# Kernel optimization log

Measured on AMD Instinct MI355X. Metric: run time of the kernel, lower is better.

## Reference

```python
import jax, jax.numpy as jnp
import numpy as np


def setup_inputs() -> dict:
    key = jax.random.key(0)
    k1, k2, k3, k4 = jax.random.split(key, 4)
    B, N, C_IN, C_OUT, K = 8, 4096, 64, 64, 16
    H = W = 64  # H * W == N
    x = jax.random.normal(k1, (B, N, C_IN), dtype=jnp.float32)
    edge_index = jax.random.randint(k2, (B, N, K), 0, N, dtype=jnp.int64)
    # 1x1 Conv2d(2*C_IN -> C_OUT) is a [C_OUT, 2*C_IN] matmul + bias
    weight = jax.random.normal(k3, (C_OUT, 2 * C_IN), dtype=jnp.float32) * 0.05
    bias = jax.random.normal(k4, (C_OUT,), dtype=jnp.float32) * 0.01
    return {"x": x, "edge_index": edge_index, "weight": weight, "bias": bias,
            "H": H, "W": W}


def reference(x, edge_index, weight, bias, H, W):
    # x: [B, N, C], edge_index: [B, N, K] with values in [0, N)
    B, N, C = x.shape
    K = edge_index.shape[-1]
    # Gather neighbor features per batch element (batched index_select)
    idx = edge_index.reshape(B, N * K, 1)                      # [B, N*K, 1]
    neighbors = jnp.take_along_axis(x, idx, axis=1)            # [B, N*K, C]
    neighbors = neighbors.reshape(B, N, K, C)                  # [B, N, K, C]
    x_central = x[:, :, None, :]                               # [B, N, 1, C]
    # edge feature: concat([x_i, x_j - x_i]) -> [B, N, K, 2C]
    edge_feat = jnp.concatenate(
        [jnp.broadcast_to(x_central, (B, N, K, C)), neighbors - x_central],
        axis=-1)
    # 1x1 conv + ReLU
    out = jax.nn.relu(jnp.einsum('bnkc,oc->bnko', edge_feat, weight) + bias)
    # max over neighbors k -> [B, N, C_out]
    out = jnp.max(out, axis=2)
    # [B, C_out, N] -> [B, C_out, H, W]
    return jnp.transpose(out, (0, 2, 1)).reshape(B, weight.shape[0], H, W)
```

## Files before the change

kernel.cpp:

```cpp
#include <hip/hip_runtime.h>
#include <stdint.h>

#define B_SZ    8
#define N_PTS   4096
#define C_IN    64
#define C_OUT   64
#define KNN     16
#define ROWS    (B_SZ * N_PTS)

typedef __attribute__((ext_vector_type(8))) short v8s;
typedef __attribute__((ext_vector_type(4))) float v4f;

__device__ inline unsigned short f2bf(float f) {
    unsigned int u = __float_as_uint(f);
    return (unsigned short)((u + 0x7FFFu + ((u >> 16) & 1u)) >> 16);
}

__global__ __launch_bounds__(256) void wprep_kernel(const float* __restrict__ w,
                                                    v8s* __restrict__ wfrag)
{
    __shared__ float wl[2 * C_IN * C_OUT];
    const int t = threadIdx.x;
    {
        const float4* src = (const float4*)w;
        float4*       dst = (float4*)wl;
#pragma unroll
        for (int i = 0; i < 8; ++i)
            dst[i * 256 + t] = src[i * 256 + t];
    }
    __syncthreads();

    const int tid  = blockIdx.x * 256 + t;
    const int lane = tid & 63;
    const int ks   = (tid >> 6) & 1;
    const int ct   = tid >> 7;
    const int col  = ct * 16 + (lane & 15);
    const int kb   = ks * 32 + 8 * (lane >> 4);

    v8s f;
#pragma unroll
    for (int j = 0; j < 8; ++j) {
        const int k = kb + j;
        const float v = (col < 64)
            ? (wl[col * 128 + k] - wl[col * 128 + 64 + k])
            : wl[(col - 64) * 128 + 64 + k];
        f[j] = (short)f2bf(v);
    }
    wfrag[tid] = f;
}

__global__ __launch_bounds__(256, 2) void proj_nbuf(
    const float* __restrict__ x,
    const v8s*  __restrict__ wfrag,
    unsigned short* __restrict__ nbuf)
{
    const int lane  = threadIdx.x & 63;
    const int wv    = threadIdx.x >> 6;
    const int batch = blockIdx.x & 7;
    const int chunk = blockIdx.x >> 3;
    const int r0    = batch * N_PTS + chunk * 64 + wv * 16;

    v8s bfrag[4][2];
#pragma unroll
    for (int ct = 0; ct < 4; ++ct)
#pragma unroll
        for (int ks = 0; ks < 2; ++ks)
            bfrag[ct][ks] = wfrag[((4 + ct) * 2 + ks) * 64 + lane];

    const int arow = r0 + (lane & 15);
    const int koff = 8 * (lane >> 4);
    v8s afrag[2];
#pragma unroll
    for (int ks = 0; ks < 2; ++ks) {
        const float* xp = x + (size_t)arow * C_IN + ks * 32 + koff;
        const float4 q0 = *(const float4*)xp;
        const float4 q1 = *(const float4*)(xp + 4);
        v8s a;
        a[0] = (short)f2bf(q0.x); a[1] = (short)f2bf(q0.y);
        a[2] = (short)f2bf(q0.z); a[3] = (short)f2bf(q0.w);
        a[4] = (short)f2bf(q1.x); a[5] = (short)f2bf(q1.y);
        a[6] = (short)f2bf(q1.z); a[7] = (short)f2bf(q1.w);
        afrag[ks] = a;
    }

    v4f acc[4];
#pragma unroll
    for (int ct = 0; ct < 4; ++ct)
        acc[ct] = (v4f){0.f, 0.f, 0.f, 0.f};

#pragma unroll
    for (int ks = 0; ks < 2; ++ks)
#pragma unroll
        for (int ct = 0; ct < 4; ++ct)
            acc[ct] = __builtin_amdgcn_mfma_f32_16x16x32_bf16(
                afrag[ks], bfrag[ct][ks], acc[ct], 0, 0, 0);

    const int crow0 = r0 + (lane >> 4) * 4;
    const int ccol  = lane & 15;
#pragma unroll
    for (int ct = 0; ct < 4; ++ct)
#pragma unroll
        for (int reg = 0; reg < 4; ++reg)
            nbuf[(size_t)(crow0 + reg) * C_OUT + ct * 16 + ccol] =
                f2bf(acc[ct][reg]);
}

#define PITCH 68

__global__ __launch_bounds__(256) void gather_fused(
    const float* __restrict__ x,
    const v8s*  __restrict__ wfrag,
    const float* __restrict__ bias,
    const int* __restrict__ eidx,
    const unsigned short* __restrict__ nbuf,
    float* __restrict__ out)
{
    __shared__ float sm[32][PITCH];

    const int t    = threadIdx.x;
    const int lane = t & 63;
    const int wv   = t >> 6;
    const int b    = blockIdx.x & 7;
    const int tn   = blockIdx.x >> 3;
    const int n0   = tn * 32;
    const int r0g  = b * N_PTS + n0;

    {
        const float4* xsrc = (const float4*)(x + (size_t)r0g * C_IN);
#pragma unroll
        for (int i = 0; i < 2; ++i) {
            const int idx = i * 256 + t;
            *(float4*)&sm[idx >> 4][(idx & 15) * 4] = xsrc[idx];
        }
    }
    __syncthreads();

    const int rq  = wv & 1;
    const int ch  = wv >> 1;
    const int rl0 = rq * 16;

    v8s bfrag[2][2];
#pragma unroll
    for (int ct = 0; ct < 2; ++ct)
#pragma unroll
        for (int ks = 0; ks < 2; ++ks)
            bfrag[ct][ks] = wfrag[((ch * 2 + ct) * 2 + ks) * 64 + lane];

    const int rl   = rl0 + (lane & 15);
    const int koff = 8 * (lane >> 4);
    v8s afrag[2];
#pragma unroll
    for (int ks = 0; ks < 2; ++ks) {
        const float* xp = &sm[rl][ks * 32 + koff];
        const float4 q0 = *(const float4*)xp;
        const float4 q1 = *(const float4*)(xp + 4);
        v8s a;
        a[0] = (short)f2bf(q0.x); a[1] = (short)f2bf(q0.y);
        a[2] = (short)f2bf(q0.z); a[3] = (short)f2bf(q0.w);
        a[4] = (short)f2bf(q1.x); a[5] = (short)f2bf(q1.y);
        a[6] = (short)f2bf(q1.z); a[7] = (short)f2bf(q1.w);
        afrag[ks] = a;
    }

    v4f acc[2];
#pragma unroll
    for (int ct = 0; ct < 2; ++ct) {
        const float bv = bias[ch * 32 + ct * 16 + (lane & 15)];
        acc[ct] = (v4f){bv, bv, bv, bv};
    }
#pragma unroll
    for (int ks = 0; ks < 2; ++ks)
#pragma unroll
        for (int ct = 0; ct < 2; ++ct)
            acc[ct] = __builtin_amdgcn_mfma_f32_16x16x32_bf16(
                afrag[ks], bfrag[ct][ks], acc[ct], 0, 0, 0);

    __syncthreads();

    const int orow = rl0 + (lane >> 4) * 4;
    const int ccol = lane & 15;
#pragma unroll
    for (int ct = 0; ct < 2; ++ct)
#pragma unroll
        for (int reg = 0; reg < 4; ++reg)
            sm[orow + reg][ch * 32 + ct * 16 + ccol] = acc[ct][reg];

    __syncthreads();

    const unsigned short* nb = nbuf + (size_t)b * N_PTS * C_OUT;
    const int o4  = (lane & 15) * 4;
    const int sub = lane >> 4;

#pragma unroll
    for (int i = 0; i < 2; ++i) {
        const int rbl   = wv * 8 + i * 4;
        const int rbase = r0g + rbl;
        int myidx = eidx[(size_t)rbase * KNN + lane] & (N_PTS - 1);

        const float4 cv = *(const float4*)&sm[rbl + sub][o4];

        float m0 = -1e30f, m1 = -1e30f, m2 = -1e30f, m3 = -1e30f;
#pragma unroll
        for (int k = 0; k < KNN; ++k) {
            const int idx = __shfl(myidx, (lane & 48) | k);
            const uint2 v = *(const uint2*)(nb + (size_t)idx * C_OUT + o4);
            m0 = fmaxf(m0, __uint_as_float(v.x << 16));
            m1 = fmaxf(m1, __uint_as_float(v.x & 0xffff0000u));
            m2 = fmaxf(m2, __uint_as_float(v.y << 16));
            m3 = fmaxf(m3, __uint_as_float(v.y & 0xffff0000u));
        }

        const int nl = rbl + sub;
        sm[nl][o4 + 0] = fmaxf(cv.x + m0, 0.f);
        sm[nl][o4 + 1] = fmaxf(cv.y + m1, 0.f);
        sm[nl][o4 + 2] = fmaxf(cv.z + m2, 0.f);
        sm[nl][o4 + 3] = fmaxf(cv.w + m3, 0.f);
    }

    __syncthreads();

    float* ob = out + (size_t)b * C_OUT * N_PTS + n0;
    const int nn = lane & 31;
    const int oh = lane >> 5;
#pragma unroll
    for (int j = 0; j < 8; ++j) {
        const int o = wv * 16 + j * 2 + oh;
        ob[(size_t)o * N_PTS + nn] = sm[nn][o];
    }
}

extern "C" void kernel_launch(void* const* d_in, const int* in_sizes, int n_in,
                              void* d_out, int out_size, void* d_ws, size_t ws_size,
                              hipStream_t stream)
{
    const float* x    = (const float*)d_in[0];
    const int*   eidx = (const int*)d_in[1];
    const float* w    = (const float*)d_in[2];
    const float* bias = (const float*)d_in[3];
    float*       out  = (float*)d_out;

    unsigned short* nbuf  = (unsigned short*)d_ws;
    v8s*            wfrag = (v8s*)((char*)d_ws + (size_t)ROWS * C_OUT * 2);

    wprep_kernel<<<4, 256, 0, stream>>>(w, wfrag);
    proj_nbuf<<<ROWS / 64, 256, 0, stream>>>(x, wfrag, nbuf);
    gather_fused<<<B_SZ * (N_PTS / 32), 256, 0, stream>>>(x, wfrag, bias, eidx,
                                                          nbuf, out);
}
```

Baseline: 20.76 us.

## Fold weight prep into consumer kernels and drop separate wprep launch

Removes the wprep kernel and has each consumer kernel load weights from global memory and build its bf16 MFMA fragments directly, including the W1-W2 subtraction in gather_fused. proj_nbuf is restructured to 32-row tiles staged through shared memory with two column tiles per wave, and launch bounds are raised to 4 blocks per SM. Edge indices are prefetched at the start of gather_fused so their latency overlaps the x tile load, and one barrier is removed. The aim is to cut one launch and its serialization, at the cost of redundant per-block weight loads and conversions.

```diff
diff --git a/kernel.cpp b/kernel.cpp
--- a/kernel.cpp
+++ b/kernel.cpp
@@ -16,100 +16,90 @@
     return (unsigned short)((u + 0x7FFFu + ((u >> 16) & 1u)) >> 16);
 }
 
-__global__ __launch_bounds__(256) void wprep_kernel(const float* __restrict__ w,
-                                                    v8s* __restrict__ wfrag)
-{
-    __shared__ float wl[2 * C_IN * C_OUT];
-    const int t = threadIdx.x;
-    {
-        const float4* src = (const float4*)w;
-        float4*       dst = (float4*)wl;
-#pragma unroll
-        for (int i = 0; i < 8; ++i)
-            dst[i * 256 + t] = src[i * 256 + t];
-    }
-    __syncthreads();
-
-    const int tid  = blockIdx.x * 256 + t;
-    const int lane = tid & 63;
-    const int ks   = (tid >> 6) & 1;
-    const int ct   = tid >> 7;
-    const int col  = ct * 16 + (lane & 15);
-    const int kb   = ks * 32 + 8 * (lane >> 4);
-
-    v8s f;
-#pragma unroll
-    for (int j = 0; j < 8; ++j) {
-        const int k = kb + j;
-        const float v = (col < 64)
-            ? (wl[col * 128 + k] - wl[col * 128 + 64 + k])
-            : wl[(col - 64) * 128 + 64 + k];
-        f[j] = (short)f2bf(v);
-    }
-    wfrag[tid] = f;
-}
-
-__global__ __launch_bounds__(256, 2) void proj_nbuf(
+__device__ inline v8s pack8(float4 q0, float4 q1) {
+    v8s a;
+    a[0] = (short)f2bf(q0.x); a[1] = (short)f2bf(q0.y);
+    a[2] = (short)f2bf(q0.z); a[3] = (short)f2bf(q0.w);
+    a[4] = (short)f2bf(q1.x); a[5] = (short)f2bf(q1.y);
+    a[6] = (short)f2bf(q1.z); a[7] = (short)f2bf(q1.w);
+    return a;
+}
+
+#define PITCH 68
+
+__global__ __launch_bounds__(256, 4) void proj_nbuf(
     const float* __restrict__ x,
-    const v8s*  __restrict__ wfrag,
+    const float* __restrict__ w,
     unsigned short* __restrict__ nbuf)
 {
-    const int lane  = threadIdx.x & 63;
-    const int wv    = threadIdx.x >> 6;
-    const int batch = blockIdx.x & 7;
-    const int chunk = blockIdx.x >> 3;
-    const int r0    = batch * N_PTS + chunk * 64 + wv * 16;
-
-    v8s bfrag[4][2];
-#pragma unroll
-    for (int ct = 0; ct < 4; ++ct)
-#pragma unroll
-        for (int ks = 0; ks < 2; ++ks)
-            bfrag[ct][ks] = wfrag[((4 + ct) * 2 + ks) * 64 + lane];
-
-    const int arow = r0 + (lane & 15);
+    __shared__ float sm[32][PITCH];
+
+    const int t    = threadIdx.x;
+    const int lane = t & 63;
+    const int wv   = t >> 6;
+    const int b    = blockIdx.x & 7;
+    const int tn   = blockIdx.x >> 3;
+    const int r0g  = b * N_PTS + tn * 32;
+
+    {
+        const float4* xsrc = (const float4*)(x + (size_t)r0g * C_IN);
+#pragma unroll
+        for (int i = 0; i < 2; ++i) {
+            const int idx = i * 256 + t;
+            *(float4*)&sm[idx >> 4][(idx & 15) * 4] = xsrc[idx];
+        }
+    }
+
+    const int rq  = wv & 1;
+    const int ch  = wv >> 1;
+    const int rl0 = rq * 16;
+
+    v8s bfrag[2][2];
+#pragma unroll
+    for (int ct = 0; ct < 2; ++ct) {
+        const int col = ch * 32 + ct * 16 + (lane & 15);
+#pragma unroll
+        for (int ks = 0; ks < 2; ++ks) {
+            const float* wp = w + col * 128 + 64 + ks * 32 + 8 * (lane >> 4);
+            bfrag[ct][ks] = pack8(*(const float4*)wp, *(const float4*)(wp + 4));
+        }
+    }
+
+    __syncthreads();
+
+    const int rl   = rl0 + (lane & 15);
     const int koff = 8 * (lane >> 4);
     v8s afrag[2];
 #pragma unroll
     for (int ks = 0; ks < 2; ++ks) {
-        const float* xp = x + (size_t)arow * C_IN + ks * 32 + koff;
-        const float4 q0 = *(const float4*)xp;
-        const float4 q1 = *(const float4*)(xp + 4);
-        v8s a;
-        a[0] = (short)f2bf(q0.x); a[1] = (short)f2bf(q0.y);
-        a[2] = (short)f2bf(q0.z); a[3] = (short)f2bf(q0.w);
-        a[4] = (short)f2bf(q1.x); a[5] = (short)f2bf(q1.y);
-        a[6] = (short)f2bf(q1.z); a[7] = (short)f2bf(q1.w);
-        afrag[ks] = a;
-    }
-
-    v4f acc[4];
-#pragma unroll
-    for (int ct = 0; ct < 4; ++ct)
+        const float* xp = &sm[rl][ks * 32 + koff];
+        afrag[ks] = pack8(*(const float4*)xp, *(const float4*)(xp + 4));
+    }
+
+    v4f acc[2];
+#pragma unroll
+    for (int ct = 0; ct < 2; ++ct)
         acc[ct] = (v4f){0.f, 0.f, 0.f, 0.f};
-
 #pragma unroll
     for (int ks = 0; ks < 2; ++ks)
 #pragma unroll
-        for (int ct = 0; ct < 4; ++ct)
+        for (int ct = 0; ct < 2; ++ct)
             acc[ct] = __builtin_amdgcn_mfma_f32_16x16x32_bf16(
                 afrag[ks], bfrag[ct][ks], acc[ct], 0, 0, 0);
 
-    const int crow0 = r0 + (lane >> 4) * 4;
-    const int ccol  = lane & 15;
-#pragma unroll
-    for (int ct = 0; ct < 4; ++ct)
+    const int orow = rl0 + (lane >> 4) * 4;
+    const int ccol = lane & 15;
+#pragma unroll
+    for (int ct = 0; ct < 2; ++ct)
 #pragma unroll
         for (int reg = 0; reg < 4; ++reg)
-            nbuf[(size_t)(crow0 + reg) * C_OUT + ct * 16 + ccol] =
+            nbuf[(size_t)(r0g + orow + reg) * C_OUT + ch * 32 + ct * 16 + ccol] =
                 f2bf(acc[ct][reg]);
 }
 
-#define PITCH 68
-
-__global__ __launch_bounds__(256) void gather_fused(
+__global__ __launch_bounds__(256, 4) void gather_fused(
     const float* __restrict__ x,
-    const v8s*  __restrict__ wfrag,
+    const float* __restrict__ w,
     const float* __restrict__ bias,
     const int* __restrict__ eidx,
     const unsigned short* __restrict__ nbuf,
@@ -125,6 +115,11 @@
     const int n0   = tn * 32;
     const int r0g  = b * N_PTS + n0;
 
+    int pidx[2];
+#pragma unroll
+    for (int i = 0; i < 2; ++i)
+        pidx[i] = eidx[(size_t)(r0g + wv * 8 + i * 4) * KNN + lane];
+
     {
         const float4* xsrc = (const float4*)(x + (size_t)r0g * C_IN);
 #pragma unroll
@@ -133,7 +128,6 @@
             *(float4*)&sm[idx >> 4][(idx & 15) * 4] = xsrc[idx];
         }
     }
-    __syncthreads();
 
     const int rq  = wv & 1;
     const int ch  = wv >> 1;
@@ -141,10 +135,22 @@
 
     v8s bfrag[2][2];
 #pragma unroll
-    for (int ct = 0; ct < 2; ++ct)
-#pragma unroll
-        for (int ks = 0; ks < 2; ++ks)
-            bfrag[ct][ks] = wfrag[((ch * 2 + ct) * 2 + ks) * 64 + lane];
+    for (int ct = 0; ct < 2; ++ct) {
+        const int col = ch * 32 + ct * 16 + (lane & 15);
+#pragma unroll
+        for (int ks = 0; ks < 2; ++ks) {
+            const float* wp = w + col * 128 + ks * 32 + 8 * (lane >> 4);
+            const float4 a0 = *(const float4*)wp;
+            const float4 a1 = *(const float4*)(wp + 4);
+            const float4 b0 = *(const float4*)(wp + 64);
+            const float4 b1 = *(const float4*)(wp + 68);
+            bfrag[ct][ks] = pack8(
+                make_float4(a0.x - b0.x, a0.y - b0.y, a0.z - b0.z, a0.w - b0.w),
+                make_float4(a1.x - b1.x, a1.y - b1.y, a1.z - b1.z, a1.w - b1.w));
+        }
+    }
+
+    __syncthreads();
 
     const int rl   = rl0 + (lane & 15);
     const int koff = 8 * (lane >> 4);
@@ -152,14 +158,7 @@
 #pragma unroll
     for (int ks = 0; ks < 2; ++ks) {
         const float* xp = &sm[rl][ks * 32 + koff];
-        const float4 q0 = *(const float4*)xp;
-        const float4 q1 = *(const float4*)(xp + 4);
-        v8s a;
-        a[0] = (short)f2bf(q0.x); a[1] = (short)f2bf(q0.y);
-        a[2] = (short)f2bf(q0.z); a[3] = (short)f2bf(q0.w);
-        a[4] = (short)f2bf(q1.x); a[5] = (short)f2bf(q1.y);
-        a[6] = (short)f2bf(q1.z); a[7] = (short)f2bf(q1.w);
-        afrag[ks] = a;
+        afrag[ks] = pack8(*(const float4*)xp, *(const float4*)(xp + 4));
     }
 
     v4f acc[2];
@@ -194,8 +193,7 @@
 #pragma unroll
     for (int i = 0; i < 2; ++i) {
         const int rbl   = wv * 8 + i * 4;
-        const int rbase = r0g + rbl;
-        int myidx = eidx[(size_t)rbase * KNN + lane] & (N_PTS - 1);
+        const int myidx = pidx[i] & (N_PTS - 1);
 
         const float4 cv = *(const float4*)&sm[rbl + sub][o4];
 
@@ -239,11 +237,8 @@
     const float* bias = (const float*)d_in[3];
     float*       out  = (float*)d_out;
 
-    unsigned short* nbuf  = (unsigned short*)d_ws;
-    v8s*            wfrag = (v8s*)((char*)d_ws + (size_t)ROWS * C_OUT * 2);
-
-    wprep_kernel<<<4, 256, 0, stream>>>(w, wfrag);
-    proj_nbuf<<<ROWS / 64, 256, 0, stream>>>(x, wfrag, nbuf);
-    gather_fused<<<B_SZ * (N_PTS / 32), 256, 0, stream>>>(x, wfrag, bias, eidx,
-                                                          nbuf, out);
-}
+    unsigned short* nbuf = (unsigned short*)d_ws;
+
+    proj_nbuf<<<ROWS / 32, 256, 0, stream>>>(x, w, nbuf);
+    gather_fused<<<ROWS / 32, 256, 0, stream>>>(x, w, bias, eidx, nbuf, out);
+}
```

Measured after the change: 25.10 us. 20.9% more time.
